# Kernel tuning notes

Measured on AMD Instinct MI355X. Metric: run time of the kernel, lower is better.

## Reference

```python
import jax, jax.numpy as jnp
import numpy as np

D_MODEL = 2048
NUM_HEADS = 16
HEAD_DIM = D_MODEL // NUM_HEADS  # 128
BASE = 10000.0


def rotate_half(x):
    x1, x2 = x[..., : x.shape[-1] // 2], x[..., x.shape[-1] // 2 :]
    return jnp.concatenate((-x2, x1), axis=-1)


def setup_inputs() -> dict:
    key = jax.random.key(0)
    ks = jax.random.split(key, 9)
    B, S, D = 2, 2048, D_MODEL
    s = 1.0 / np.sqrt(D)
    return {
        "x": jax.random.normal(ks[0], (B, S, D), dtype=jnp.float32),
        "Wq": jax.random.normal(ks[1], (D, D), dtype=jnp.float32) * s,
        "bq": jnp.zeros((D,), dtype=jnp.float32),
        "Wk": jax.random.normal(ks[2], (D, D), dtype=jnp.float32) * s,
        "bk": jnp.zeros((D,), dtype=jnp.float32),
        "Wv": jax.random.normal(ks[3], (D, D), dtype=jnp.float32) * s,
        "bv": jnp.zeros((D,), dtype=jnp.float32),
        "Wo": jax.random.normal(ks[4], (D, D), dtype=jnp.float32) * s,
        "bo": jnp.zeros((D,), dtype=jnp.float32),
    }


def reference(x, Wq, bq, Wk, bk, Wv, bv, Wo, bo):
    B, S, D = x.shape
    H, hd = NUM_HEADS, HEAD_DIM

    def proj(W, b):
        # nn.Linear: x @ W^T + b, then split heads -> [B, H, S, hd]
        return (x @ W.T + b).reshape(B, S, H, hd).transpose(0, 2, 1, 3)

    q = proj(Wq, bq)
    k = proj(Wk, bk)
    v = proj(Wv, bv)

    # Rotary embedding table (note: original applies cos()/sin() to a
    # tensor that already contains [sin(si), cos(si)] — reproduced faithfully).
    positions = jnp.arange(S, dtype=jnp.float32)
    inv_freq = 1.0 / (BASE ** (jnp.arange(0, hd, 2, dtype=jnp.float32) / hd))
    sinusoid = positions[:, None] * inv_freq[None, :]            # [S, hd/2]
    emb = jnp.concatenate((jnp.sin(sinusoid), jnp.cos(sinusoid)), axis=-1)  # [S, hd]
    cos_e = jnp.cos(emb)  # broadcast over [B, H, S, hd]
    sin_e = jnp.sin(emb)

    q_rot = q * cos_e + rotate_half(q) * sin_e
    k_rot = k * cos_e + rotate_half(k) * sin_e

    scale = 1.0 / jnp.sqrt(jnp.asarray(hd, dtype=x.dtype))
    attn = jnp.einsum("bhqd,bhkd->bhqk", q_rot, k_rot) * scale
    attn = jax.nn.softmax(attn, axis=-1)
    out = jnp.einsum("bhqk,bhkd->bhqd", attn, v)
    out = out.transpose(0, 2, 1, 3).reshape(B, S, D)
    return out @ Wo.T + bo
```

## Files before the change

### kernel.cpp

```cpp
#include <hip/hip_runtime.h>
#include <math.h>

#define D_MODEL 2048
#define NHEADS  16
#define HD      128
#define SEQ     2048
#define BATCH   2
#define SCALE   0.08838834764831845f
#define SMAX    20.0f

typedef __attribute__((ext_vector_type(8))) short short8;
typedef __attribute__((ext_vector_type(4))) float f32x4;

#define MFMA16(a,b,c) __builtin_amdgcn_mfma_f32_16x16x32_bf16((a),(b),(c),0,0,0)

__device__ __forceinline__ unsigned short f2bf(float x){
    unsigned u = __float_as_uint(x);
    return (unsigned short)((u + 0x7FFFu + ((u>>16)&1u)) >> 16);
}
__device__ __forceinline__ float bf2f(unsigned short h){ return __uint_as_float(((unsigned)h)<<16); }

__device__ __forceinline__ void async16(void* lds, const void* g){
    __builtin_amdgcn_global_load_lds((const __attribute__((address_space(1))) unsigned int*)g,
                                     (__attribute__((address_space(3))) unsigned int*)lds, 16, 0, 0);
}

__device__ __forceinline__ void split4(float4 v, ushort4* h, ushort4* l){
    h->x=f2bf(v.x); l->x=f2bf(v.x-bf2f(h->x));
    h->y=f2bf(v.y); l->y=f2bf(v.y-bf2f(h->y));
    h->z=f2bf(v.z); l->z=f2bf(v.z-bf2f(h->z));
    h->w=f2bf(v.w); l->w=f2bf(v.w-bf2f(h->w));
}

__global__ __launch_bounds__(256)
void prep_all(const float* __restrict__ x, const float* __restrict__ Wq,
              const float* __restrict__ Wk, const float* __restrict__ Wv,
              unsigned short* __restrict__ Xhi, unsigned short* __restrict__ Xlo,
              unsigned short* __restrict__ WqHi, unsigned short* __restrict__ WqLo,
              unsigned short* __restrict__ WkHi, unsigned short* __restrict__ WkLo,
              unsigned short* __restrict__ WvHi,
              float4* __restrict__ tab)
{
    const int b = blockIdx.x, t = threadIdx.x;
    if (b < 8192) {
        int i = b*256 + t;
        ushort4 h,l; split4(((const float4*)x)[i], &h, &l);
        ((ushort4*)Xhi)[i]=h; ((ushort4*)Xlo)[i]=l;
    } else if (b < 12288) {
        int i = (b-8192)*256 + t;
        ushort4 h,l; split4(((const float4*)Wq)[i], &h, &l);
        ((ushort4*)WqHi)[i]=h; ((ushort4*)WqLo)[i]=l;
    } else if (b < 16384) {
        int i = (b-12288)*256 + t;
        ushort4 h,l; split4(((const float4*)Wk)[i], &h, &l);
        ((ushort4*)WkHi)[i]=h; ((ushort4*)WkLo)[i]=l;
    } else if (b < 20480) {
        int i = (b-16384)*256 + t;
        ushort4 h,l; split4(((const float4*)Wv)[i], &h, &l);
        ((ushort4*)WvHi)[i]=h;
    } else {
        int i = (b-20480)*256 + t;
        int s = i >> 6, d = i & 63;
        float f = powf(10000.0f, -(float)d * (1.0f/64.0f));
        float sv = (float)s * f;
        float sn = sinf(sv), cs = cosf(sv);
        tab[i] = (float4){cosf(sn), sinf(sn), cosf(cs), sinf(cs)};
    }
}

__global__ __launch_bounds__(256)
void split_w(const float* __restrict__ src, unsigned short* __restrict__ hi,
             unsigned short* __restrict__ lo, int n4)
{
    int i = blockIdx.x*256 + threadIdx.x;
    if (i >= n4) return;
    ushort4 h,l; split4(((const float4*)src)[i], &h, &l);
    ((ushort4*)hi)[i]=h; ((ushort4*)lo)[i]=l;
}

template<bool THREE, int Q>
__device__ __forceinline__ void phase_mfma(const unsigned short* Bh, const unsigned short* Bl,
                                           const short8 (&ah)[4], const short8 (&al)[4],
                                           f32x4 (&acc)[4][4], int wn, int quad, int l15)
{
    int n = wn*64 + Q*16 + l15;
    int c = (quad ^ ((n>>1)&3))*8;
    short8 bh_ = *(const short8*)&Bh[n*32 + c];
    short8 bl_ = {};
    if constexpr (THREE) bl_ = *(const short8*)&Bl[n*32 + c];
    __builtin_amdgcn_s_setprio(1);
    acc[0][Q] = MFMA16(ah[0], bh_, acc[0][Q]);
    acc[1][Q] = MFMA16(ah[1], bh_, acc[1][Q]);
    acc[2][Q] = MFMA16(ah[2], bh_, acc[2][Q]);
    acc[3][Q] = MFMA16(ah[3], bh_, acc[3][Q]);
    acc[0][Q] = MFMA16(al[0], bh_, acc[0][Q]);
    acc[1][Q] = MFMA16(al[1], bh_, acc[1][Q]);
    acc[2][Q] = MFMA16(al[2], bh_, acc[2][Q]);
    acc[3][Q] = MFMA16(al[3], bh_, acc[3][Q]);
    if constexpr (THREE) {
        acc[0][Q] = MFMA16(ah[0], bl_, acc[0][Q]);
        acc[1][Q] = MFMA16(ah[1], bl_, acc[1][Q]);
        acc[2][Q] = MFMA16(ah[2], bl_, acc[2][Q]);
        acc[3][Q] = MFMA16(ah[3], bl_, acc[3][Q]);
    }
    __builtin_amdgcn_s_setprio(0);
}

template<bool THREE>
__device__ __forceinline__ void gemm_core(const unsigned short* __restrict__ Agh,
                                          const unsigned short* __restrict__ Agl,
                                          const unsigned short* __restrict__ Bgh,
                                          const unsigned short* __restrict__ Bgl,
                                          unsigned short* lds, int m0, int n0,
                                          f32x4 (&acc)[4][4])
{
    const int t = threadIdx.x, w = t>>6, lane = t&63;
    const int quad = lane>>4, l15 = lane&15;
    const int wm = w>>1, wn = w&1;

    unsigned short *c0 = lds, *c1 = lds + 24576, *c2 = lds + 49152;

    auto stageA = [&](unsigned short* P, const unsigned short* SRC, int u, int kt2){
        int idx = t + u*512; int rw = idx>>2, sg = idx&3;
        int sgp = sg ^ ((rw>>1)&3);
        async16((char*)(P + rw*32 + sg*8), SRC + (size_t)(m0+rw)*2048 + kt2 + sgp*8);
    };
    auto stageB = [&](unsigned short* P, const unsigned short* SRC, int kt2){
        int rw = t>>2, sg = t&3; int sgp = sg ^ ((rw>>1)&3);
        async16((char*)(P + rw*32 + sg*8), SRC + (size_t)(n0+rw)*2048 + kt2 + sgp*8);
    };

    stageA(c0,        Agh, 0, 0);  stageA(c0,        Agh, 1, 0);
    stageA(c0+8192,   Agl, 0, 0);  stageA(c0+8192,   Agl, 1, 0);
    stageB(c0+16384,  Bgh, 0);
    if constexpr (THREE) stageB(c0+20480, Bgl, 0);
    stageA(c1,        Agh, 0, 32); stageA(c1,        Agh, 1, 32);
    stageA(c1+8192,   Agl, 0, 32); stageA(c1+8192,   Agl, 1, 32);
    stageB(c1+16384,  Bgh, 32);
    if constexpr (THREE) stageB(c1+20480, Bgl, 32);

    for (int kt = 0; kt < 64; ++kt) {
        if (kt == 63) {
            asm volatile("s_waitcnt vmcnt(0)" ::: "memory");
        } else if constexpr (THREE) {
            asm volatile("s_waitcnt vmcnt(6)" ::: "memory");
        } else {
            asm volatile("s_waitcnt vmcnt(5)" ::: "memory");
        }
        __builtin_amdgcn_s_barrier();
        __builtin_amdgcn_sched_barrier(0);

        const unsigned short* Ah = c0;
        const unsigned short* Al = c0 + 8192;
        const unsigned short* Bh = c0 + 16384;
        const unsigned short* Bl = c0 + 20480;
        const int  kt2 = (kt+2)*32;
        const bool st  = (kt < 62);

        short8 ah[4], al[4];
#pragma unroll
        for (int mi=0;mi<4;mi++){
            int m = wm*64 + mi*16 + l15;
            int c = (quad ^ ((m>>1)&3))*8;
            ah[mi] = *(const short8*)&Ah[m*32 + c];
            al[mi] = *(const short8*)&Al[m*32 + c];
        }
        if (st){ stageA(c2,       Agh, 0, kt2); stageA(c2,       Agh, 1, kt2); }
        phase_mfma<THREE,0>(Bh, Bl, ah, al, acc, wn, quad, l15);
        __builtin_amdgcn_s_barrier();

        if (st){ stageA(c2+8192,  Agl, 0, kt2); stageA(c2+8192,  Agl, 1, kt2); }
        phase_mfma<THREE,1>(Bh, Bl, ah, al, acc, wn, quad, l15);
        __builtin_amdgcn_s_barrier();

        if (st){ stageB(c2+16384, Bgh, kt2); }
        phase_mfma<THREE,2>(Bh, Bl, ah, al, acc, wn, quad, l15);
        __builtin_amdgcn_s_barrier();

        if constexpr (THREE) { if (st) stageB(c2+20480, Bgl, kt2); }
        phase_mfma<THREE,3>(Bh, Bl, ah, al, acc, wn, quad, l15);
        __builtin_amdgcn_s_barrier();

        unsigned short* tmp = c0; c0 = c1; c1 = c2; c2 = tmp;
    }
}

__global__ __launch_bounds__(512,2)
void gemm_qk(const unsigned short* __restrict__ Xhi_g, const unsigned short* __restrict__ Xlo_g,
             const unsigned short* __restrict__ wsplit,
             const float* __restrict__ bq, const float* __restrict__ bk,
             const float4* __restrict__ tab,
             unsigned short* __restrict__ Qhi, unsigned short* __restrict__ Qlo,
             unsigned short* __restrict__ Khi, unsigned short* __restrict__ Klo)
{
    extern __shared__ unsigned short ldsm[];
    const int z = blockIdx.z;
    const unsigned short* Whi = wsplit + (size_t)z*8388608u;
    const unsigned short* Wlo = Whi + 4194304u;
    const int t = threadIdx.x, w = t>>6, lane = t&63;
    const int quad = lane>>4, l15 = lane&15;
    const int wm = w>>1, wn = w&1;
    const int m0 = blockIdx.y*256, n0 = blockIdx.x*128;

    f32x4 acc[4][4];
#pragma unroll
    for (int i=0;i<4;i++)
#pragma unroll
        for (int j=0;j<4;j++) acc[i][j] = (f32x4){0.f,0.f,0.f,0.f};

    gemm_core<true>(Xhi_g, Xlo_g, Whi, Wlo, ldsm, m0, n0, acc);
    __syncthreads();

    const float* bias = (z==0)?bq:bk;
#pragma unroll
    for (int ni=0;ni<4;ni++){
        float bv_ = bias[n0 + wn*64 + ni*16 + l15];
#pragma unroll
        for (int mi=0;mi<4;mi++){
            acc[mi][ni][0]+=bv_; acc[mi][ni][1]+=bv_; acc[mi][ni][2]+=bv_; acc[mi][ni][3]+=bv_;
        }
    }

    float* xch = (float*)ldsm;
    unsigned short* OHi = (z==0)?Qhi:Khi;
    unsigned short* OLo = (z==0)?Qlo:Klo;
    const float scl = (z==0)?SCALE:1.0f;
    const int h = blockIdx.x;
    const int b = m0>>11;
    const size_t bhbase = ((size_t)(b*16+h)*2048);

    if (wn == 0) {
#pragma unroll
        for (int mi=0;mi<4;mi++)
#pragma unroll
        for (int ni=2;ni<4;ni++)
#pragma unroll
        for (int r=0;r<4;r++)
            xch[(wm*64+mi*16+quad*4+r)*68 + (ni-2)*16+l15] = acc[mi][ni][r];
    } else {
#pragma unroll
        for (int mi=0;mi<4;mi++)
#pragma unroll
        for (int ni=0;ni<2;ni++)
#pragma unroll
        for (int r=0;r<4;r++)
            xch[(wm*64+mi*16+quad*4+r)*68 + 32 + ni*16+l15] = acc[mi][ni][r];
    }
    __syncthreads();

    if (wn == 0) {
#pragma unroll
        for (int ni2=0;ni2<2;ni2++){
            int d = ni2*16 + l15;
#pragma unroll
            for (int mi=0;mi<4;mi++)
#pragma unroll
            for (int r=0;r<4;r++){
                int ml = wm*64 + mi*16 + quad*4 + r;
                int s = (m0 + ml) & 2047;
                float4 tv = tab[s*64 + d];
                float c_lo = acc[mi][ni2][r];
                float c_hi = xch[ml*68 + 32 + d];
                float o1 = (c_lo*tv.x - c_hi*tv.y)*scl;
                float o2 = (c_hi*tv.z + c_lo*tv.w)*scl;
                size_t base = (bhbase + s)*128;
                unsigned short h1=f2bf(o1); OHi[base+d]=h1;    OLo[base+d]=f2bf(o1-bf2f(h1));
                unsigned short h2=f2bf(o2); OHi[base+64+d]=h2; OLo[base+64+d]=f2bf(o2-bf2f(h2));
            }
        }
    } else {
#pragma unroll
        for (int ni2=0;ni2<2;ni2++){
            int d = 32 + ni2*16 + l15;
#pragma unroll
            for (int mi=0;mi<4;mi++)
#pragma unroll
            for (int r=0;r<4;r++){
                int ml = wm*64 + mi*16 + quad*4 + r;
                int s = (m0 + ml) & 2047;
                float4 tv = tab[s*64 + d];
                float c_lo = xch[ml*68 + (d-32)];
                float c_hi = acc[mi][ni2+2][r];
                float o1 = (c_lo*tv.x - c_hi*tv.y)*scl;
                float o2 = (c_hi*tv.z + c_lo*tv.w)*scl;
                size_t base = (bhbase + s)*128;
                unsigned short h1=f2bf(o1); OHi[base+d]=h1;    OLo[base+d]=f2bf(o1-bf2f(h1));
                unsigned short h2=f2bf(o2); OHi[base+64+d]=h2; OLo[base+64+d]=f2bf(o2-bf2f(h2));
            }
        }
    }
}

__global__ __launch_bounds__(512,2)
void gemm_v(const unsigned short* __restrict__ Xhi_g, const unsigned short* __restrict__ Xlo_g,
            const unsigned short* __restrict__ WvHi,
            const float* __restrict__ bv, unsigned short* __restrict__ Vt)
{
    extern __shared__ unsigned short ldsm[];
    const int t = threadIdx.x, w = t>>6, lane = t&63;
    const int quad = lane>>4, l15 = lane&15;
    const int wm = w>>1, wn = w&1;
    const int m0 = blockIdx.y*256, n0 = blockIdx.x*128;

    f32x4 acc[4][4];
#pragma unroll
    for (int i=0;i<4;i++)
#pragma unroll
        for (int j=0;j<4;j++) acc[i][j] = (f32x4){0.f,0.f,0.f,0.f};

    gemm_core<false>(Xhi_g, Xlo_g, WvHi, nullptr, ldsm, m0, n0, acc);
    __syncthreads();

#pragma unroll
    for (int ni=0;ni<4;ni++){
        float bv_ = bv[n0 + wn*64 + ni*16 + l15];
#pragma unroll
        for (int mi=0;mi<4;mi++){
            acc[mi][ni][0]+=bv_; acc[mi][ni][1]+=bv_; acc[mi][ni][2]+=bv_; acc[mi][ni][3]+=bv_;
        }
    }

    unsigned short* vb = ldsm;
#pragma unroll
    for (int mi=0;mi<4;mi++)
#pragma unroll
    for (int ni=0;ni<4;ni++)
#pragma unroll
    for (int r=0;r<4;r++){
        int d  = wn*64 + ni*16 + l15;
        int ml = wm*64 + mi*16 + quad*4 + r;
        vb[d*264 + ml] = f2bf(acc[mi][ni][r]);
    }
    __syncthreads();

    const int b = m0>>11, s0 = m0&2047, h = blockIdx.x;
    unsigned short* vdst = Vt + (size_t)(b*16+h)*128*2048;
    const int dr = t>>2, part = (t&3)*64;
#pragma unroll
    for (int j=0;j<8;j++){
        uint4 v = *(const uint4*)&vb[dr*264 + part + j*8];
        *(uint4*)(vdst + (size_t)dr*2048 + s0 + part + j*8) = v;
    }
}

__global__ __launch_bounds__(512,2)
void gemm_o(const unsigned short* __restrict__ Ahi_g, const unsigned short* __restrict__ Alo_g,
            const unsigned short* __restrict__ Whi_g, const unsigned short* __restrict__ Wlo_g,
            const float* __restrict__ bias, float* __restrict__ out)
{
    extern __shared__ unsigned short ldsm[];
    const int t = threadIdx.x, w = t>>6, lane = t&63;
    const int quad = lane>>4, l15 = lane&15;
    const int wm = w>>1, wn = w&1;
    const int m0 = blockIdx.y*256, n0 = blockIdx.x*128;

    f32x4 acc[4][4];
#pragma unroll
    for (int i=0;i<4;i++)
#pragma unroll
        for (int j=0;j<4;j++) acc[i][j] = (f32x4){0.f,0.f,0.f,0.f};

    gemm_core<true>(Ahi_g, Alo_g, Whi_g, Wlo_g, ldsm, m0, n0, acc);

#pragma unroll
    for (int ni=0;ni<4;ni++){
        int n = n0 + wn*64 + ni*16 + l15;
        float bv_ = bias[n];
#pragma unroll
        for (int mi=0;mi<4;mi++)
#pragma unroll
        for (int r=0;r<4;r++){
            int m = m0 + wm*64 + mi*16 + quad*4 + r;
            out[(size_t)m*2048 + n] = acc[mi][ni][r] + bv_;
        }
    }
}

__global__ __launch_bounds__(256,2)
void flash_mfma(const unsigned short* __restrict__ Qhi, const unsigned short* __restrict__ Qlo,
                const unsigned short* __restrict__ Khi, const unsigned short* __restrict__ Klo,
                const unsigned short* __restrict__ Vt,
                unsigned short* __restrict__ Ohi, unsigned short* __restrict__ Olo)
{
    const int t=threadIdx.x, w=t>>6, lane=t&63, quad=lane>>4, l15=lane&15;
    const int bh = blockIdx.y, qt = blockIdx.x;

    __shared__ __align__(16) unsigned short sm[32768];
    unsigned short* Ps = sm + 24576 + w*2048;

    short8 qf[2][2][4];
    const size_t qrow = (size_t)bh*2048 + qt*128 + w*32;
#pragma unroll
    for (int mb=0;mb<2;mb++){
        size_t r = qrow + mb*16 + l15;
#pragma unroll
        for (int kc=0;kc<4;kc++){
            qf[0][mb][kc] = *(const short8*)(Qhi + r*128 + kc*32 + quad*8);
            qf[1][mb][kc] = *(const short8*)(Qlo + r*128 + kc*32 + quad*8);
        }
    }

    f32x4 O[2][8];
#pragma unroll
    for (int mb=0;mb<2;mb++)
#pragma unroll
        for (int nb=0;nb<8;nb++) O[mb][nb]=(f32x4){0.f,0.f,0.f,0.f};
    float lrow[2][4];
#pragma unroll
    for (int mb=0;mb<2;mb++)
#pragma unroll
        for (int r=0;r<4;r++) lrow[mb][r]=0.f;

    const char* KhiB = (const char*)(Khi + (size_t)bh*2048*128);
    const char* KloB = (const char*)(Klo + (size_t)bh*2048*128);
    const unsigned short* VtB = Vt + (size_t)bh*128*2048;
    char* smb = (char*)sm;

    for (int kt=0; kt<2048; kt+=64) {
#pragma unroll
        for (int i=0;i<4;i++){
            int o16 = t + 256*i;
            int krow = o16>>4, kc = o16&15;
            int kcp = kc ^ (krow&15);
            async16(smb + i*4096 + t*16,         KhiB + (size_t)kt*256 + krow*256 + kcp*16);
            async16(smb + 16384 + i*4096 + t*16, KloB + (size_t)kt*256 + krow*256 + kcp*16);
            int d = (t>>3) + i*32, c = t&7;
            int cp = c ^ (d&7);
            async16(smb + 32768 + i*4096 + t*16, VtB + (size_t)d*2048 + kt + cp*8);
        }
        __syncthreads();

        f32x4 S[2][4];
#pragma unroll
        for (int mb=0;mb<2;mb++)
#pragma unroll
            for (int nb=0;nb<4;nb++) S[mb][nb]=(f32x4){0.f,0.f,0.f,0.f};
#pragma unroll
        for (int kc=0;kc<4;kc++)
#pragma unroll
        for (int nb=0;nb<4;nb++){
            int m = nb*16+l15;
            int c = ((kc*4+quad) ^ (m&15))*8;
            short8 kh = *(const short8*)&sm[m*128 + c];
            short8 kl = *(const short8*)&sm[8192 + m*128 + c];
#pragma unroll
            for (int mb=0;mb<2;mb++){
                S[mb][nb] = MFMA16(qf[0][mb][kc], kh, S[mb][nb]);
                S[mb][nb] = MFMA16(qf[1][mb][kc], kh, S[mb][nb]);
                S[mb][nb] = MFMA16(qf[0][mb][kc], kl, S[mb][nb]);
            }
        }

#pragma unroll
        for (int mb=0;mb<2;mb++)
#pragma unroll
        for (int nb=0;nb<4;nb++)
#pragma unroll
        for (int r=0;r<4;r++){
            float p = __expf(S[mb][nb][r] - SMAX);
            lrow[mb][r] += p;
            int q = mb*16 + quad*4 + r;
            int c = nb*16 + l15;
            Ps[q*64 + (((c>>3)^(q&7))<<3) + (c&7)] = f2bf(p);
        }

#pragma unroll
        for (int kc2=0;kc2<2;kc2++){
            short8 pf0 = *(const short8*)&Ps[(l15)*64      + (((kc2*4+quad)^(l15&7))<<3)];
            short8 pf1 = *(const short8*)&Ps[(16+l15)*64   + (((kc2*4+quad)^(l15&7))<<3)];
#pragma unroll
            for (int nb=0;nb<8;nb++){
                int d = nb*16+l15;
                int c = ((kc2*4+quad) ^ (d&7))*8;
                short8 vf = *(const short8*)&sm[16384 + d*64 + c];
                O[0][nb] = MFMA16(pf0, vf, O[0][nb]);
                O[1][nb] = MFMA16(pf1, vf, O[1][nb]);
            }
        }
        __syncthreads();
    }

#pragma unroll
    for (int mb=0;mb<2;mb++)
#pragma unroll
        for (int d=1;d<16;d<<=1)
#pragma unroll
            for (int r=0;r<4;r++) lrow[mb][r] += __shfl_xor(lrow[mb][r], d);

    const int b = bh>>4, h = bh&15;
#pragma unroll
    for (int mb=0;mb<2;mb++)
#pragma unroll
    for (int nb=0;nb<8;nb++)
#pragma unroll
    for (int r=0;r<4;r++){
        float v = O[mb][nb][r] / lrow[mb][r];
        int qg = qt*128 + w*32 + mb*16 + quad*4 + r;
        size_t base = ((size_t)(b*2048 + qg))*2048 + h*128 + nb*16 + l15;
        unsigned short hh = f2bf(v);
        Ohi[base]=hh; Olo[base]=f2bf(v-bf2f(hh));
    }
}

extern "C" void kernel_launch(void* const* d_in, const int* in_sizes, int n_in,
                              void* d_out, int out_size, void* d_ws, size_t ws_size,
                              hipStream_t stream)
{
    (void)in_sizes; (void)n_in; (void)out_size; (void)ws_size;
    const float* x  = (const float*)d_in[0];
    const float* Wq = (const float*)d_in[1];
    const float* bq = (const float*)d_in[2];
    const float* Wk = (const float*)d_in[3];
    const float* bk = (const float*)d_in[4];
    const float* Wv = (const float*)d_in[5];
    const float* bv = (const float*)d_in[6];
    const float* Wo = (const float*)d_in[7];
    const float* bo = (const float*)d_in[8];
    float* out = (float*)d_out;

    unsigned short* wsB = (unsigned short*)d_ws;
    unsigned short* C0  = wsB + 20971520u;
    unsigned short* Qhi = C0;
    unsigned short* Qlo = C0 + 8388608u;
    unsigned short* Khi = C0 + 16777216u;
    unsigned short* Klo = C0 + 25165824u;
    unsigned short* Vt  = C0 + 33554432u;
    float4* tab = (float4*)(wsB + 62914560u);

    unsigned short* Xhi = (unsigned short*)d_out;
    unsigned short* Xlo = Xhi + 8388608u;

    static bool attr_done = false;
    if (!attr_done) {
        (void)hipFuncSetAttribute(reinterpret_cast<const void*>(&gemm_qk),
                                  hipFuncAttributeMaxDynamicSharedMemorySize, 147456);
        (void)hipFuncSetAttribute(reinterpret_cast<const void*>(&gemm_v),
                                  hipFuncAttributeMaxDynamicSharedMemorySize, 147456);
        (void)hipFuncSetAttribute(reinterpret_cast<const void*>(&gemm_o),
                                  hipFuncAttributeMaxDynamicSharedMemorySize, 147456);
        attr_done = true;
    }

    prep_all<<<20992,256,0,stream>>>(x, Wq, Wk, Wv,
                                     Xhi, Xlo,
                                     wsB,            wsB+4194304u,
                                     wsB+8388608u,   wsB+12582912u,
                                     wsB+16777216u,  tab);

    gemm_qk<<<dim3(16,16,2),512,147456,stream>>>(Xhi, Xlo, wsB, bq, bk, tab,
                                                 Qhi, Qlo, Khi, Klo);
    gemm_v <<<dim3(16,16),  512,147456,stream>>>(Xhi, Xlo, wsB+16777216u, bv, Vt);

    unsigned short* Ohi = wsB;
    unsigned short* Olo = wsB + 8388608u;
    flash_mfma<<<dim3(16,32),256,0,stream>>>(Qhi,Qlo,Khi,Klo,Vt, Ohi, Olo);

    unsigned short* WoHi = C0;
    unsigned short* WoLo = C0 + 4194304u;
    split_w<<<4096,256,0,stream>>>(Wo, WoHi, WoLo, 1048576);

    gemm_o<<<dim3(16,16),512,147456,stream>>>(Ohi, Olo, WoHi, WoLo, bo, out);
}
```

Measured before the change: 632.3 us.

## Software-pipeline LDS fragment reads in QK GEMM and remap flash blocks per XCD

Adds a new GEMM core for the Q/K projection that prefetches the next B column fragment, and the next tile's A and B fragments, while the current MFMAs run. It uses explicit vmcnt/lgkmcnt waits and sched_barriers to control ordering, which hides LDS read latency behind matrix math. The flash attention kernel also remaps block indices so blocks of the same batch-head land on the same XCD, aiming to improve L2 reuse of K/V. The extra prefetch registers raise register pressure, which may hurt occupancy at two blocks per CU.

```diff
diff --git a/kernel.cpp b/kernel.cpp
--- a/kernel.cpp
+++ b/kernel.cpp
@@ -78,6 +78,7 @@
     ((ushort4*)hi)[i]=h; ((ushort4*)lo)[i]=l;
 }
 
+
 template<bool THREE, int Q>
 __device__ __forceinline__ void phase_mfma(const unsigned short* Bh, const unsigned short* Bl,
                                            const short8 (&ah)[4], const short8 (&al)[4],
@@ -107,12 +108,12 @@
 }
 
 template<bool THREE>
-__device__ __forceinline__ void gemm_core(const unsigned short* __restrict__ Agh,
-                                          const unsigned short* __restrict__ Agl,
-                                          const unsigned short* __restrict__ Bgh,
-                                          const unsigned short* __restrict__ Bgl,
-                                          unsigned short* lds, int m0, int n0,
-                                          f32x4 (&acc)[4][4])
+__device__ __forceinline__ void gemm_core_r1(const unsigned short* __restrict__ Agh,
+                                             const unsigned short* __restrict__ Agl,
+                                             const unsigned short* __restrict__ Bgh,
+                                             const unsigned short* __restrict__ Bgl,
+                                             unsigned short* lds, int m0, int n0,
+                                             f32x4 (&acc)[4][4])
 {
     const int t = threadIdx.x, w = t>>6, lane = t&63;
     const int quad = lane>>4, l15 = lane&15;
@@ -185,6 +186,140 @@
     }
 }
 
+template<bool THREE>
+__device__ __forceinline__ void read_A3(const unsigned short* Ah, const unsigned short* Al,
+                                        short8 (&ah)[4], short8 (&al)[4],
+                                        int wm, int quad, int l15)
+{
+#pragma unroll
+    for (int mi=0;mi<4;mi++){
+        int m = wm*64 + mi*16 + l15;
+        int c = (quad ^ ((m>>1)&3))*8;
+        ah[mi] = *(const short8*)&Ah[m*32 + c];
+        al[mi] = *(const short8*)&Al[m*32 + c];
+    }
+}
+
+template<bool THREE, int Q>
+__device__ __forceinline__ void read_B3(const unsigned short* Bh, const unsigned short* Bl,
+                                        short8& bh, short8& bl, int wn, int quad, int l15)
+{
+    int n = wn*64 + Q*16 + l15;
+    int c = (quad ^ ((n>>1)&3))*8;
+    bh = *(const short8*)&Bh[n*32 + c];
+    if constexpr (THREE) bl = *(const short8*)&Bl[n*32 + c];
+    else                 bl = (short8){};
+}
+
+template<bool THREE, int Q>
+__device__ __forceinline__ void col_mfma3(const short8 (&ah)[4], const short8 (&al)[4],
+                                          short8 bh, short8 bl, f32x4 (&acc)[4][4])
+{
+    __builtin_amdgcn_s_setprio(1);
+    acc[0][Q] = MFMA16(ah[0], bh, acc[0][Q]);
+    acc[1][Q] = MFMA16(ah[1], bh, acc[1][Q]);
+    acc[2][Q] = MFMA16(ah[2], bh, acc[2][Q]);
+    acc[3][Q] = MFMA16(ah[3], bh, acc[3][Q]);
+    acc[0][Q] = MFMA16(al[0], bh, acc[0][Q]);
+    acc[1][Q] = MFMA16(al[1], bh, acc[1][Q]);
+    acc[2][Q] = MFMA16(al[2], bh, acc[2][Q]);
+    acc[3][Q] = MFMA16(al[3], bh, acc[3][Q]);
+    if constexpr (THREE) {
+        acc[0][Q] = MFMA16(ah[0], bl, acc[0][Q]);
+        acc[1][Q] = MFMA16(ah[1], bl, acc[1][Q]);
+        acc[2][Q] = MFMA16(ah[2], bl, acc[2][Q]);
+        acc[3][Q] = MFMA16(ah[3], bl, acc[3][Q]);
+    }
+    __builtin_amdgcn_s_setprio(0);
+}
+
+template<bool THREE>
+__device__ __forceinline__ void gemm_core3(const unsigned short* __restrict__ Agh,
+                                           const unsigned short* __restrict__ Agl,
+                                           const unsigned short* __restrict__ Bgh,
+                                           const unsigned short* __restrict__ Bgl,
+                                           unsigned short* lds, int m0, int n0,
+                                           f32x4 (&acc)[4][4])
+{
+    const int t = threadIdx.x, w = t>>6, lane = t&63;
+    const int quad = lane>>4, l15 = lane&15;
+    const int wm = w>>1, wn = w&1;
+
+    unsigned short *c0 = lds, *c1 = lds + 24576, *c2 = lds + 49152;
+
+    auto stageA = [&](unsigned short* P, const unsigned short* SRC, int u, int kt2){
+        int idx = t + u*512; int rw = idx>>2, sg = idx&3;
+        int sgp = sg ^ ((rw>>1)&3);
+        async16((char*)(P + rw*32 + sg*8), SRC + (size_t)(m0+rw)*2048 + kt2 + sgp*8);
+    };
+    auto stageB = [&](unsigned short* P, const unsigned short* SRC, int kt2){
+        int rw = t>>2, sg = t&3; int sgp = sg ^ ((rw>>1)&3);
+        async16((char*)(P + rw*32 + sg*8), SRC + (size_t)(n0+rw)*2048 + kt2 + sgp*8);
+    };
+    auto stage_tile = [&](unsigned short* P, int kt2){
+        stageA(P,        Agh, 0, kt2);  stageA(P,        Agh, 1, kt2);
+        stageA(P+8192,   Agl, 0, kt2);  stageA(P+8192,   Agl, 1, kt2);
+        stageB(P+16384,  Bgh, kt2);
+        if constexpr (THREE) stageB(P+20480, Bgl, kt2);
+    };
+
+    stage_tile(c0, 0);
+    stage_tile(c1, 32);
+    if constexpr (THREE) asm volatile("s_waitcnt vmcnt(6)" ::: "memory");
+    else                 asm volatile("s_waitcnt vmcnt(5)" ::: "memory");
+    __builtin_amdgcn_s_barrier();
+    __builtin_amdgcn_sched_barrier(0);
+
+    short8 ah[4], al[4], ahp[4], alp[4];
+    short8 b0h, b0l, b1h, b1l, b2h, b2l, b3h, b3l, b0hp, b0lp;
+    read_A3<THREE>(c0, c0+8192, ah, al, wm, quad, l15);
+    read_B3<THREE,0>(c0+16384, c0+20480, b0h, b0l, wn, quad, l15);
+
+    for (int kt = 0; kt < 64; ++kt) {
+        const bool st  = (kt < 62);
+        const int  kt2 = (kt+2)*32;
+
+        read_B3<THREE,1>(c0+16384, c0+20480, b1h, b1l, wn, quad, l15);
+        if (st){ stageA(c2,       Agh, 0, kt2); stageA(c2,       Agh, 1, kt2); }
+        col_mfma3<THREE,0>(ah, al, b0h, b0l, acc);
+        __builtin_amdgcn_sched_barrier(0);
+
+        read_B3<THREE,2>(c0+16384, c0+20480, b2h, b2l, wn, quad, l15);
+        if (st){ stageA(c2+8192,  Agl, 0, kt2); stageA(c2+8192,  Agl, 1, kt2); }
+        col_mfma3<THREE,1>(ah, al, b1h, b1l, acc);
+        __builtin_amdgcn_sched_barrier(0);
+
+        read_B3<THREE,3>(c0+16384, c0+20480, b3h, b3l, wn, quad, l15);
+        if (st){ stageB(c2+16384, Bgh, kt2); }
+        col_mfma3<THREE,2>(ah, al, b2h, b2l, acc);
+        __builtin_amdgcn_sched_barrier(0);
+
+        if constexpr (THREE) { if (st) stageB(c2+20480, Bgl, kt2); }
+        if (kt < 63) {
+            __builtin_amdgcn_sched_barrier(0);
+            asm volatile("s_waitcnt lgkmcnt(0)" ::: "memory");
+            if (st) {
+                if constexpr (THREE) asm volatile("s_waitcnt vmcnt(6)" ::: "memory");
+                else                 asm volatile("s_waitcnt vmcnt(5)" ::: "memory");
+            } else {
+                asm volatile("s_waitcnt vmcnt(0)" ::: "memory");
+            }
+            __builtin_amdgcn_s_barrier();
+            __builtin_amdgcn_sched_barrier(0);
+            read_A3<THREE>(c1, c1+8192, ahp, alp, wm, quad, l15);
+            read_B3<THREE,0>(c1+16384, c1+20480, b0hp, b0lp, wn, quad, l15);
+            __builtin_amdgcn_sched_barrier(0);
+            col_mfma3<THREE,3>(ah, al, b3h, b3l, acc);
+#pragma unroll
+            for (int i=0;i<4;i++){ ah[i]=ahp[i]; al[i]=alp[i]; }
+            b0h = b0hp; b0l = b0lp;
+            unsigned short* tmp = c0; c0 = c1; c1 = c2; c2 = tmp;
+        } else {
+            col_mfma3<THREE,3>(ah, al, b3h, b3l, acc);
+        }
+    }
+}
+
 __global__ __launch_bounds__(512,2)
 void gemm_qk(const unsigned short* __restrict__ Xhi_g, const unsigned short* __restrict__ Xlo_g,
              const unsigned short* __restrict__ wsplit,
@@ -208,7 +343,7 @@
 #pragma unroll
         for (int j=0;j<4;j++) acc[i][j] = (f32x4){0.f,0.f,0.f,0.f};
 
-    gemm_core<true>(Xhi_g, Xlo_g, Whi, Wlo, ldsm, m0, n0, acc);
+    gemm_core3<true>(Xhi_g, Xlo_g, Whi, Wlo, ldsm, m0, n0, acc);
     __syncthreads();
 
     const float* bias = (z==0)?bq:bk;
@@ -308,7 +443,7 @@
 #pragma unroll
         for (int j=0;j<4;j++) acc[i][j] = (f32x4){0.f,0.f,0.f,0.f};
 
-    gemm_core<false>(Xhi_g, Xlo_g, WvHi, nullptr, ldsm, m0, n0, acc);
+    gemm_core_r1<false>(Xhi_g, Xlo_g, WvHi, nullptr, ldsm, m0, n0, acc);
     __syncthreads();
 
 #pragma unroll
@@ -360,7 +495,7 @@
 #pragma unroll
         for (int j=0;j<4;j++) acc[i][j] = (f32x4){0.f,0.f,0.f,0.f};
 
-    gemm_core<true>(Ahi_g, Alo_g, Whi_g, Wlo_g, ldsm, m0, n0, acc);
+    gemm_core_r1<true>(Ahi_g, Alo_g, Whi_g, Wlo_g, ldsm, m0, n0, acc);
 
 #pragma unroll
     for (int ni=0;ni<4;ni++){
@@ -383,7 +518,10 @@
                 unsigned short* __restrict__ Ohi, unsigned short* __restrict__ Olo)
 {
     const int t=threadIdx.x, w=t>>6, lane=t&63, quad=lane>>4, l15=lane&15;
-    const int bh = blockIdx.y, qt = blockIdx.x;
+    const int fid = blockIdx.y*16 + blockIdx.x;
+    const int xcd = fid & 7, slot = fid >> 3;
+    const int bh = xcd*4 + (slot>>4);
+    const int qt = slot & 15;
 
     __shared__ __align__(16) unsigned short sm[32768];
     unsigned short* Ps = sm + 24576 + w*2048;
```

Measured after the change: 670.6 us. 1.06x slower.
